# Kernel optimization log

Measured on AMD Instinct MI355X. Metric: run time of the kernel, lower is better.

The kernel has to match this reference:

```python
import jax, jax.numpy as jnp
import numpy as np

B, NQ, NK, QS, KS, H, VD = 16, 64, 512, 256, 256, 256, 256


def setup_inputs() -> dict:
    key = jax.random.key(0)
    k1, k2, k3, k4, k5, k6, k7 = jax.random.split(key, 7)
    return {
        "queries": jax.random.normal(k1, (B, NQ, QS), dtype=jnp.float32),
        "keys": jax.random.normal(k2, (B, NK, KS), dtype=jnp.float32),
        "values": jax.random.normal(k3, (B, NK, VD), dtype=jnp.float32),
        "valid_lens": jax.random.randint(k4, (B,), 1, NK + 1, dtype=jnp.int32),
        # learned params (nn.Linear with bias=False): W_q [QS,H], W_k [KS,H], w_v [H]
        "W_q": jax.random.normal(k5, (QS, H), dtype=jnp.float32) / np.sqrt(QS),
        "W_k": jax.random.normal(k6, (KS, H), dtype=jnp.float32) / np.sqrt(KS),
        "w_v": jax.random.normal(k7, (H,), dtype=jnp.float32) / np.sqrt(H),
    }


def reference(queries, keys, values, valid_lens, W_q, W_k, w_v):
    # project: q [B,nq,H], k [B,nk,H]
    q = jnp.einsum("bqd,dh->bqh", queries, W_q)
    k = jnp.einsum("bkd,dh->bkh", keys, W_k)
    # broadcast-add -> tanh -> score reduction via w_v: [B,nq,nk]
    features = jnp.tanh(q[:, :, None, :] + k[:, None, :, :])  # [B,nq,nk,H]
    scores = jnp.einsum("bqkh,h->bqk", features, w_v)
    # masked softmax over keys (positions >= valid_len masked out)
    mask = jnp.arange(scores.shape[-1])[None, None, :] < valid_lens[:, None, None]
    scores = jnp.where(mask, scores, -1e6)
    attn = jax.nn.softmax(scores, axis=-1)
    # weighted sum of values (dropout p=0 / eval mode => identity)
    return jnp.einsum("bqk,bkv->bqv", attn, values)
```

## Files before the change

kernel.cpp:

```cpp
#include <hip/hip_runtime.h>
#include <hip/hip_bf16.h>

#define BB 16
#define NQ 64
#define NK 512
#define HD 256

typedef __attribute__((ext_vector_type(8))) short short8;
typedef __attribute__((ext_vector_type(4))) float f32x4;

__device__ __forceinline__ ushort bf16_rne(float v) {
    unsigned u = __float_as_uint(v);
    return (ushort)((u + 0x7FFFu + ((u >> 16) & 1u)) >> 16);
}
__device__ __forceinline__ float bf16_to_f(ushort h) {
    return __uint_as_float(((unsigned)h) << 16);
}

__global__ __launch_bounds__(256) void convert_split(
    const float* __restrict__ q, const float* __restrict__ k,
    const float* __restrict__ wq, const float* __restrict__ wk,
    ushort* __restrict__ qh, ushort* __restrict__ ql,
    ushort* __restrict__ kh, ushort* __restrict__ kl,
    ushort* __restrict__ wqh, ushort* __restrict__ wql,
    ushort* __restrict__ wkh, ushort* __restrict__ wkl)
{
    const int idx = blockIdx.x * 256 + threadIdx.x;
    if (blockIdx.x < 2304) {
        int e = idx * 4;
        const float* src; ushort *dh, *dl; int off;
        if (e < 1024 * 256) { src = q; dh = qh; dl = ql; off = e; }
        else { src = k; dh = kh; dl = kl; off = e - 1024 * 256; }
        float4 v = *(const float4*)&src[off];
        float fv[4] = {v.x, v.y, v.z, v.w};
        ushort hh[4], ll[4];
        #pragma unroll
        for (int c = 0; c < 4; ++c) {
            hh[c] = bf16_rne(fv[c]);
            ll[c] = bf16_rne(fv[c] - bf16_to_f(hh[c]));
        }
        *(ushort4*)&dh[off] = make_ushort4(hh[0], hh[1], hh[2], hh[3]);
        *(ushort4*)&dl[off] = make_ushort4(ll[0], ll[1], ll[2], ll[3]);
    } else {
        int widx = idx - 2304 * 256;
        const float* W; ushort *wh, *wl;
        if (widx < 16384) { W = wq; wh = wqh; wl = wql; }
        else { W = wk; wh = wkh; wl = wkl; widx -= 16384; }
        int n  = widx >> 6;
        int k4 = (widx & 63) * 4;
        ushort hh[4], ll[4];
        #pragma unroll
        for (int c = 0; c < 4; ++c) {
            float v = W[(k4 + c) * 256 + n];
            hh[c] = bf16_rne(v);
            ll[c] = bf16_rne(v - bf16_to_f(hh[c]));
        }
        *(ushort4*)&wh[n * 256 + k4] = make_ushort4(hh[0], hh[1], hh[2], hh[3]);
        *(ushort4*)&wl[n * 256 + k4] = make_ushort4(ll[0], ll[1], ll[2], ll[3]);
    }
}

__global__ __launch_bounds__(256, 2) void proj_mfma2(
    const ushort* __restrict__ qh, const ushort* __restrict__ ql,
    const ushort* __restrict__ kh, const ushort* __restrict__ kl,
    const ushort* __restrict__ wqh, const ushort* __restrict__ wql,
    const ushort* __restrict__ wkh, const ushort* __restrict__ wkl,
    float* __restrict__ qp, float* __restrict__ kp, float scale)
{
    __shared__ ushort AsH[128 * 64], AsL[128 * 64];
    __shared__ ushort BsH[64 * 64],  BsL[64 * 64];

    const ushort *Ah, *Al, *Bh, *Bl; float* C; int rows0;
    if (blockIdx.x < 8) { Ah = qh; Al = ql; Bh = wqh; Bl = wql; C = qp; rows0 = blockIdx.x * 128; }
    else                { Ah = kh; Al = kl; Bh = wkh; Bl = wkl; C = kp; rows0 = (blockIdx.x - 8) * 128; }
    const int cols0 = blockIdx.y * 64;

    const int t = threadIdx.x, lane = t & 63, wave = t >> 6;
    const int quad = lane >> 4, l15 = lane & 15;
    const int lr = lane >> 3;
    const int cg = (lane & 7) ^ lr;
    const int swz0 = quad ^ (l15 & 7);
    const int swz1 = (quad + 4) ^ (l15 & 7);

    f32x4 acc[2][4];
    #pragma unroll
    for (int i = 0; i < 2; ++i)
        #pragma unroll
        for (int j = 0; j < 4; ++j)
            acc[i][j] = (f32x4){0.f, 0.f, 0.f, 0.f};

    short8 rAh[4], rAl[4], rBh[2], rBl[2];
    #pragma unroll
    for (int i = 0; i < 4; ++i) {
        size_t g = (size_t)(rows0 + (wave * 4 + i) * 8 + lr) * 256 + cg * 8;
        rAh[i] = *(const short8*)&Ah[g];
        rAl[i] = *(const short8*)&Al[g];
    }
    #pragma unroll
    for (int j = 0; j < 2; ++j) {
        size_t g = (size_t)(cols0 + (wave * 2 + j) * 8 + lr) * 256 + cg * 8;
        rBh[j] = *(const short8*)&Bh[g];
        rBl[j] = *(const short8*)&Bl[g];
    }

    for (int k0 = 0; k0 < 256; k0 += 64) {
        __syncthreads();
        #pragma unroll
        for (int i = 0; i < 4; ++i) {
            int ci = (wave * 4 + i) * 64 + lane;
            *(short8*)&AsH[ci * 8] = rAh[i];
            *(short8*)&AsL[ci * 8] = rAl[i];
        }
        #pragma unroll
        for (int j = 0; j < 2; ++j) {
            int ci = (wave * 2 + j) * 64 + lane;
            *(short8*)&BsH[ci * 8] = rBh[j];
            *(short8*)&BsL[ci * 8] = rBl[j];
        }
        __syncthreads();

        if (k0 + 64 < 256) {
            #pragma unroll
            for (int i = 0; i < 4; ++i) {
                size_t g = (size_t)(rows0 + (wave * 4 + i) * 8 + lr) * 256 + k0 + 64 + cg * 8;
                rAh[i] = *(const short8*)&Ah[g];
                rAl[i] = *(const short8*)&Al[g];
            }
            #pragma unroll
            for (int j = 0; j < 2; ++j) {
                size_t g = (size_t)(cols0 + (wave * 2 + j) * 8 + lr) * 256 + k0 + 64 + cg * 8;
                rBh[j] = *(const short8*)&Bh[g];
                rBl[j] = *(const short8*)&Bl[g];
            }
        }

        #pragma unroll
        for (int ks = 0; ks < 2; ++ks) {
            const int s = ks ? swz1 : swz0;
            short8 aH[2], aL[2], bH[4], bL[4];
            #pragma unroll
            for (int ms = 0; ms < 2; ++ms) {
                int r = wave * 32 + ms * 16 + l15;
                aH[ms] = *(const short8*)&AsH[r * 64 + s * 8];
                aL[ms] = *(const short8*)&AsL[r * 64 + s * 8];
            }
            #pragma unroll
            for (int ns = 0; ns < 4; ++ns) {
                int n = ns * 16 + l15;
                bH[ns] = *(const short8*)&BsH[n * 64 + s * 8];
                bL[ns] = *(const short8*)&BsL[n * 64 + s * 8];
            }
            #pragma unroll
            for (int ms = 0; ms < 2; ++ms)
                #pragma unroll
                for (int ns = 0; ns < 4; ++ns)
                    acc[ms][ns] = __builtin_amdgcn_mfma_f32_16x16x32_bf16(aH[ms], bH[ns], acc[ms][ns], 0, 0, 0);
            #pragma unroll
            for (int ms = 0; ms < 2; ++ms)
                #pragma unroll
                for (int ns = 0; ns < 4; ++ns)
                    acc[ms][ns] = __builtin_amdgcn_mfma_f32_16x16x32_bf16(aL[ms], bH[ns], acc[ms][ns], 0, 0, 0);
            #pragma unroll
            for (int ms = 0; ms < 2; ++ms)
                #pragma unroll
                for (int ns = 0; ns < 4; ++ns)
                    acc[ms][ns] = __builtin_amdgcn_mfma_f32_16x16x32_bf16(aH[ms], bL[ns], acc[ms][ns], 0, 0, 0);
        }
    }

    #pragma unroll
    for (int ms = 0; ms < 2; ++ms) {
        int rbase = rows0 + wave * 32 + ms * 16 + quad * 4;
        #pragma unroll
        for (int ns = 0; ns < 4; ++ns) {
            int col = cols0 + ns * 16 + l15;
            #pragma unroll
            for (int r = 0; r < 4; ++r)
                C[(size_t)(rbase + r) * 256 + col] = acc[ms][ns][r] * scale;
        }
    }
}

__global__ __launch_bounds__(256, 2) void attn_kernel(
    const float* __restrict__ qp,
    const float* __restrict__ kp,
    const float* __restrict__ values,
    const int*   __restrict__ vlens,
    const float* __restrict__ w_v,
    float* __restrict__ out)
{
    __shared__ float q_s[2][HD];
    __shared__ float wv_s[HD];
    __shared__ float sc[2][NK];
    __shared__ float part[4][2][HD];
    __shared__ float redm[4], reds[4], invs[2];

    const int b     = blockIdx.x & 15;
    const int qpair = blockIdx.x >> 4;
    const int qi0   = qpair * 2;
    const int t     = threadIdx.x;
    const int lane  = t & 63;
    const int wave  = t >> 6;
    const int vl    = vlens[b];
    const int vla   = (vl + 15) & ~15;
    const size_t row0 = (size_t)b * NQ + qi0;

    q_s[0][t] = qp[row0 * HD + t];
    q_s[1][t] = qp[(row0 + 1) * HD + t];
    wv_s[t]   = w_v[t];
    __syncthreads();

    float Wsum;
    {
        float ws = wv_s[lane] + wv_s[lane + 64] + wv_s[lane + 128] + wv_s[lane + 192];
        #pragma unroll
        for (int off = 32; off; off >>= 1) ws += __shfl_xor(ws, off);
        Wsum = ws;
    }

    const int keyLoc = lane >> 4;
    const int ch     = lane & 15;
    float4 qa[4], qb[4], wf[4];
    #pragma unroll
    for (int m = 0; m < 4; ++m) {
        qa[m] = *(const float4*)&q_s[0][ch * 4 + m * 64];
        qb[m] = *(const float4*)&q_s[1][ch * 4 + m * 64];
        wf[m] = *(const float4*)&wv_s[ch * 4 + m * 64];
    }

    const float* kbase = kp + (size_t)b * NK * HD;
    const float* kptr  = kbase + (size_t)(wave * 4 + keyLoc) * HD + ch * 4;

    float4 kk[4];
    #pragma unroll
    for (int m = 0; m < 4; ++m) kk[m] = *(const float4*)(kptr + m * 64);

    for (int nb = wave * 4; nb < vla; nb += 16) {
        float4 kn[4];
        #pragma unroll
        for (int m = 0; m < 4; ++m) kn[m] = *(const float4*)(kptr + 16 * HD + m * 64);

        float p0 = 0.f, p1 = 0.f;
        #pragma unroll
        for (int m = 0; m < 4; ++m) {
            float kv[4]  = {kk[m].x, kk[m].y, kk[m].z, kk[m].w};
            float qav[4] = {qa[m].x, qa[m].y, qa[m].z, qa[m].w};
            float qbv[4] = {qb[m].x, qb[m].y, qb[m].z, qb[m].w};
            float wv4[4] = {wf[m].x, wf[m].y, wf[m].z, wf[m].w};
            #pragma unroll
            for (int c = 0; c < 4; ++c) {
                float r0 = __builtin_amdgcn_rcpf(__builtin_amdgcn_exp2f(qav[c] + kv[c]) + 1.f);
                float r1 = __builtin_amdgcn_rcpf(__builtin_amdgcn_exp2f(qbv[c] + kv[c]) + 1.f);
                p0 = fmaf(wv4[c], r0, p0);
                p1 = fmaf(wv4[c], r1, p1);
            }
        }
        p0 += __shfl_down(p0, 8); p0 += __shfl_down(p0, 4);
        p0 += __shfl_down(p0, 2); p0 += __shfl_down(p0, 1);
        p1 += __shfl_down(p1, 8); p1 += __shfl_down(p1, 4);
        p1 += __shfl_down(p1, 2); p1 += __shfl_down(p1, 1);
        if (ch == 0) {
            sc[0][nb + keyLoc] = fmaf(-2.f, p0, Wsum);
            sc[1][nb + keyLoc] = fmaf(-2.f, p1, Wsum);
        }
        #pragma unroll
        for (int m = 0; m < 4; ++m) kk[m] = kn[m];
        kptr += 16 * HD;
    }
    __syncthreads();

    {
        const int qq  = wave >> 1;
        const int sub = wave & 1;
        float m = -1e30f;
        for (int n = sub * 64 + lane; n < vl; n += 128) m = fmaxf(m, sc[qq][n]);
        #pragma unroll
        for (int off = 32; off; off >>= 1) m = fmaxf(m, __shfl_xor(m, off));
        if (lane == 0) redm[wave] = m;
        __syncthreads();
        m = fmaxf(redm[qq * 2], redm[qq * 2 + 1]);

        float ssum = 0.f;
        const float L2E = 1.4426950408889634f;
        for (int n = sub * 64 + lane; n < vl; n += 128) {
            float p = __builtin_amdgcn_exp2f((sc[qq][n] - m) * L2E);
            sc[qq][n] = p;
            ssum += p;
        }
        #pragma unroll
        for (int off = 32; off; off >>= 1) ssum += __shfl_xor(ssum, off);
        if (lane == 0) reds[wave] = ssum;
        if (vl + t < vla) { sc[0][vl + t] = 0.f; sc[1][vl + t] = 0.f; }
        __syncthreads();
        if (t == 0)  invs[0] = __builtin_amdgcn_rcpf(reds[0] + reds[1]);
        if (t == 64) invs[1] = __builtin_amdgcn_rcpf(reds[2] + reds[3]);
    }
    __syncthreads();

    float4 acc0 = {0.f, 0.f, 0.f, 0.f};
    float4 acc1 = {0.f, 0.f, 0.f, 0.f};
    const float* vbase = values + (size_t)b * NK * HD;
    for (int nb = wave * 4; nb < vla; nb += 16) {
        float4 v[4]; float pa[4], pb[4];
        #pragma unroll
        for (int u = 0; u < 4; ++u) {
            v[u]  = *(const float4*)&vbase[(size_t)(nb + u) * HD + lane * 4];
            pa[u] = sc[0][nb + u];
            pb[u] = sc[1][nb + u];
        }
        #pragma unroll
        for (int u = 0; u < 4; ++u) {
            acc0.x = fmaf(pa[u], v[u].x, acc0.x);
            acc0.y = fmaf(pa[u], v[u].y, acc0.y);
            acc0.z = fmaf(pa[u], v[u].z, acc0.z);
            acc0.w = fmaf(pa[u], v[u].w, acc0.w);
            acc1.x = fmaf(pb[u], v[u].x, acc1.x);
            acc1.y = fmaf(pb[u], v[u].y, acc1.y);
            acc1.z = fmaf(pb[u], v[u].z, acc1.z);
            acc1.w = fmaf(pb[u], v[u].w, acc1.w);
        }
    }
    *(float4*)&part[wave][0][lane * 4] = acc0;
    *(float4*)&part[wave][1][lane * 4] = acc1;
    __syncthreads();

    if (wave < 2) {
        float4 p0 = *(const float4*)&part[0][wave][lane * 4];
        float4 p1 = *(const float4*)&part[1][wave][lane * 4];
        float4 p2 = *(const float4*)&part[2][wave][lane * 4];
        float4 p3 = *(const float4*)&part[3][wave][lane * 4];
        const float inv = invs[wave];
        float4 o;
        o.x = ((p0.x + p1.x) + (p2.x + p3.x)) * inv;
        o.y = ((p0.y + p1.y) + (p2.y + p3.y)) * inv;
        o.z = ((p0.z + p1.z) + (p2.z + p3.z)) * inv;
        o.w = ((p0.w + p1.w) + (p2.w + p3.w)) * inv;
        *(float4*)&out[(row0 + wave) * HD + lane * 4] = o;
    }
}

extern "C" void kernel_launch(void* const* d_in, const int* in_sizes, int n_in,
                              void* d_out, int out_size, void* d_ws, size_t ws_size,
                              hipStream_t stream) {
    const float* queries = (const float*)d_in[0];
    const float* keys    = (const float*)d_in[1];
    const float* values  = (const float*)d_in[2];
    const int*   vlens   = (const int*)d_in[3];
    const float* W_q     = (const float*)d_in[4];
    const float* W_k     = (const float*)d_in[5];
    const float* w_v     = (const float*)d_in[6];
    float* out = (float*)d_out;

    float*  kp  = (float*)d_ws;
    ushort* qh  = (ushort*)((char*)d_ws + (8 << 20));
    ushort* ql  = qh  + 1024 * 256;
    ushort* kh  = ql  + 1024 * 256;
    ushort* kl  = kh  + 8192 * 256;
    ushort* wqh = kl  + 8192 * 256;
    ushort* wql = wqh + 65536;
    ushort* wkh = wql + 65536;
    ushort* wkl = wkh + 65536;

    float* qp = out;

    const float SC = 2.885390081777927f;

    convert_split<<<dim3(2432), 256, 0, stream>>>(queries, keys, W_q, W_k,
                                                  qh, ql, kh, kl,
                                                  wqh, wql, wkh, wkl);
    proj_mfma2<<<dim3(72, 4), 256, 0, stream>>>(qh, ql, kh, kl,
                                                wqh, wql, wkh, wkl,
                                                qp, kp, SC);
    attn_kernel<<<dim3(512), 256, 0, stream>>>(qp, kp, values, vlens, w_v, out);
}
```

Before: 119.6 us.

## Split fused attention into tiled score kernel and separate softmax-PV kernel

The score computation moves out of the per-query-pair attention kernel into its own kernel. Each block of that kernel stages 32 queries and 16 keys in shared memory, so each key row is reused across many queries and the 3D grid skips chunks beyond the valid length. Scores go through a global workspace buffer, and a second kernel does the masked softmax and value weighting. This trades an extra launch plus a global round-trip of the score matrix for better key reuse and more parallelism in the tanh-dominated stage.

```diff
diff --git a/kernel.cpp b/kernel.cpp
--- a/kernel.cpp
+++ b/kernel.cpp
@@ -181,16 +181,91 @@
     }
 }
 
-__global__ __launch_bounds__(256, 2) void attn_kernel(
+__global__ __launch_bounds__(256) void score_kernel(
     const float* __restrict__ qp,
     const float* __restrict__ kp,
+    const int*   __restrict__ vlens,
+    const float* __restrict__ w_v,
+    float* __restrict__ S)
+{
+    __shared__ float qs[32][260];
+    __shared__ float ks[16][260];
+    __shared__ float wv[HD];
+
+    const int b     = blockIdx.x;
+    const int chunk = blockIdx.y;
+    const int qhalf = blockIdx.z;
+    const int vl    = vlens[b];
+    if (chunk * 16 >= vl) return;
+
+    const int t    = threadIdx.x;
+    const int lane = t & 63;
+    const int wave = t >> 6;
+
+    const float* qsrc = qp + ((size_t)b * NQ + qhalf * 32) * HD;
+    #pragma unroll
+    for (int i = 0; i < 8; ++i) {
+        int idx = i * 256 + t;
+        int row = idx >> 6, c4 = (idx & 63) * 4;
+        *(float4*)&qs[row][c4] = *(const float4*)&qsrc[(size_t)row * HD + c4];
+    }
+    const float* ksrc = kp + ((size_t)b * NK + chunk * 16) * HD;
+    #pragma unroll
+    for (int i = 0; i < 4; ++i) {
+        int idx = i * 256 + t;
+        int row = idx >> 6, c4 = (idx & 63) * 4;
+        *(float4*)&ks[row][c4] = *(const float4*)&ksrc[(size_t)row * HD + c4];
+    }
+    if (t < 64) *(float4*)&wv[t * 4] = *(const float4*)&w_v[t * 4];
+    __syncthreads();
+
+    float Wsum;
+    {
+        float ws = wv[lane] + wv[lane + 64] + wv[lane + 128] + wv[lane + 192];
+        #pragma unroll
+        for (int off = 32; off; off >>= 1) ws += __shfl_xor(ws, off);
+        Wsum = ws;
+    }
+
+    const int qloc = wave * 8 + (lane >> 3);
+    const int n0   = (lane & 7) * 2;
+
+    const float* qrow = &qs[qloc][0];
+    const float* k0   = &ks[n0][0];
+    const float* k1   = &ks[n0 + 1][0];
+
+    float s0 = 0.f, s1 = 0.f;
+    #pragma unroll 8
+    for (int h4 = 0; h4 < 64; ++h4) {
+        float4 q4 = *(const float4*)&qrow[h4 * 4];
+        float4 w4 = *(const float4*)&wv[h4 * 4];
+        float4 ka = *(const float4*)&k0[h4 * 4];
+        float4 kb = *(const float4*)&k1[h4 * 4];
+        float qv[4] = {q4.x, q4.y, q4.z, q4.w};
+        float wv4[4] = {w4.x, w4.y, w4.z, w4.w};
+        float kav[4] = {ka.x, ka.y, ka.z, ka.w};
+        float kbv[4] = {kb.x, kb.y, kb.z, kb.w};
+        #pragma unroll
+        for (int c = 0; c < 4; ++c) {
+            float r0 = __builtin_amdgcn_rcpf(__builtin_amdgcn_exp2f(qv[c] + kav[c]) + 1.f);
+            float r1 = __builtin_amdgcn_rcpf(__builtin_amdgcn_exp2f(qv[c] + kbv[c]) + 1.f);
+            s0 = fmaf(wv4[c], r0, s0);
+            s1 = fmaf(wv4[c], r1, s1);
+        }
+    }
+    float2 o;
+    o.x = fmaf(-2.f, s0, Wsum);
+    o.y = fmaf(-2.f, s1, Wsum);
+    const int qg = qhalf * 32 + qloc;
+    *(float2*)&S[((size_t)b * NQ + qg) * NK + chunk * 16 + n0] = o;
+}
+
+__global__ __launch_bounds__(256, 2) void softmax_pv(
+    const float* __restrict__ S,
     const float* __restrict__ values,
     const int*   __restrict__ vlens,
-    const float* __restrict__ w_v,
     float* __restrict__ out)
 {
-    __shared__ float q_s[2][HD];
-    __shared__ float wv_s[HD];
     __shared__ float sc[2][NK];
     __shared__ float part[4][2][HD];
     __shared__ float redm[4], reds[4], invs[2];
@@ -205,68 +280,9 @@
     const int vla   = (vl + 15) & ~15;
     const size_t row0 = (size_t)b * NQ + qi0;
 
-    q_s[0][t] = qp[row0 * HD + t];
-    q_s[1][t] = qp[(row0 + 1) * HD + t];
-    wv_s[t]   = w_v[t];
-    __syncthreads();
-
-    float Wsum;
-    {
-        float ws = wv_s[lane] + wv_s[lane + 64] + wv_s[lane + 128] + wv_s[lane + 192];
-        #pragma unroll
-        for (int off = 32; off; off >>= 1) ws += __shfl_xor(ws, off);
-        Wsum = ws;
-    }
-
-    const int keyLoc = lane >> 4;
-    const int ch     = lane & 15;
-    float4 qa[4], qb[4], wf[4];
-    #pragma unroll
-    for (int m = 0; m < 4; ++m) {
-        qa[m] = *(const float4*)&q_s[0][ch * 4 + m * 64];
-        qb[m] = *(const float4*)&q_s[1][ch * 4 + m * 64];
-        wf[m] = *(const float4*)&wv_s[ch * 4 + m * 64];
-    }
-
-    const float* kbase = kp + (size_t)b * NK * HD;
-    const float* kptr  = kbase + (size_t)(wave * 4 + keyLoc) * HD + ch * 4;
-
-    float4 kk[4];
-    #pragma unroll
-    for (int m = 0; m < 4; ++m) kk[m] = *(const float4*)(kptr + m * 64);
-
-    for (int nb = wave * 4; nb < vla; nb += 16) {
-        float4 kn[4];
-        #pragma unroll
-        for (int m = 0; m < 4; ++m) kn[m] = *(const float4*)(kptr + 16 * HD + m * 64);
-
-        float p0 = 0.f, p1 = 0.f;
-        #pragma unroll
-        for (int m = 0; m < 4; ++m) {
-            float kv[4]  = {kk[m].x, kk[m].y, kk[m].z, kk[m].w};
-            float qav[4] = {qa[m].x, qa[m].y, qa[m].z, qa[m].w};
-            float qbv[4] = {qb[m].x, qb[m].y, qb[m].z, qb[m].w};
-            float wv4[4] = {wf[m].x, wf[m].y, wf[m].z, wf[m].w};
-            #pragma unroll
-            for (int c = 0; c < 4; ++c) {
-                float r0 = __builtin_amdgcn_rcpf(__builtin_amdgcn_exp2f(qav[c] + kv[c]) + 1.f);
-                float r1 = __builtin_amdgcn_rcpf(__builtin_amdgcn_exp2f(qbv[c] + kv[c]) + 1.f);
-                p0 = fmaf(wv4[c], r0, p0);
-                p1 = fmaf(wv4[c], r1, p1);
-            }
-        }
-        p0 += __shfl_down(p0, 8); p0 += __shfl_down(p0, 4);
-        p0 += __shfl_down(p0, 2); p0 += __shfl_down(p0, 1);
-        p1 += __shfl_down(p1, 8); p1 += __shfl_down(p1, 4);
-        p1 += __shfl_down(p1, 2); p1 += __shfl_down(p1, 1);
-        if (ch == 0) {
-            sc[0][nb + keyLoc] = fmaf(-2.f, p0, Wsum);
-            sc[1][nb + keyLoc] = fmaf(-2.f, p1, Wsum);
-        }
-        #pragma unroll
-        for (int m = 0; m < 4; ++m) kk[m] = kn[m];
-        kptr += 16 * HD;
-    }
+    const float* S0 = &S[row0 * NK];
+    const float* S1 = &S[(row0 + 1) * NK];
+    for (int n = t; n < vla; n += 256) { sc[0][n] = S0[n]; sc[1][n] = S1[n]; }
     __syncthreads();
 
     {
@@ -352,7 +368,9 @@
     float* out = (float*)d_out;
 
     float*  kp  = (float*)d_ws;
-    ushort* qh  = (ushort*)((char*)d_ws + (8 << 20));
+    float*  qp  = kp + (size_t)BB * NK * HD;
+    float*  S   = qp + (size_t)BB * NQ * HD;
+    ushort* qh  = (ushort*)(S + (size_t)BB * NQ * NK);
     ushort* ql  = qh  + 1024 * 256;
     ushort* kh  = ql  + 1024 * 256;
     ushort* kl  = kh  + 8192 * 256;
@@ -361,8 +379,6 @@
     ushort* wkh = wql + 65536;
     ushort* wkl = wkh + 65536;
 
-    float* qp = out;
-
     const float SC = 2.885390081777927f;
 
     convert_split<<<dim3(2432), 256, 0, stream>>>(queries, keys, W_q, W_k,
@@ -371,5 +387,6 @@
     proj_mfma2<<<dim3(72, 4), 256, 0, stream>>>(qh, ql, kh, kl,
                                                 wqh, wql, wkh, wkl,
                                                 qp, kp, SC);
-    attn_kernel<<<dim3(512), 256, 0, stream>>>(qp, kp, values, vlens, w_v, out);
-}
+    score_kernel<<<dim3(16, 32, 2), 256, 0, stream>>>(qp, kp, vlens, w_v, S);
+    softmax_pv<<<dim3(512), 256, 0, stream>>>(S, values, vlens, out);
+}
```

New measurement: 127.6 us. 1.07x slower.

## Split attention over key segments with split-K softmax combine kernel

Applied to the files above, without the earlier changes.

The single attention kernel becomes two. The first computes scores, a local softmax and the P·V product for each 64-key segment, launching grid (512,8) and skipping segments beyond valid_len. A second kernel merges the per-segment max, sum and partial outputs into the final result. The score math also precomputes exp2(q) once and uses exp2(q)*exp2(k) per element, which removes one add per element but keeps the exp of k per pair. The aim is more parallelism and an even load across blocks with varying valid_len, at the cost of an extra launch and a round trip of the partial outputs through memory.

```diff
diff --git a/kernel.cpp b/kernel.cpp
--- a/kernel.cpp
+++ b/kernel.cpp
@@ -181,147 +181,122 @@
     }
 }
 
-__global__ __launch_bounds__(256, 2) void attn_kernel(
+__global__ __launch_bounds__(256) void score_pv_seg(
     const float* __restrict__ qp,
     const float* __restrict__ kp,
     const float* __restrict__ values,
     const int*   __restrict__ vlens,
     const float* __restrict__ w_v,
-    float* __restrict__ out)
+    float* __restrict__ pO,
+    float* __restrict__ pM,
+    float* __restrict__ pL)
 {
-    __shared__ float q_s[2][HD];
-    __shared__ float wv_s[HD];
-    __shared__ float sc[2][NK];
+    __shared__ float Ps[2][64];
     __shared__ float part[4][2][HD];
-    __shared__ float redm[4], reds[4], invs[2];
 
     const int b     = blockIdx.x & 15;
     const int qpair = blockIdx.x >> 4;
-    const int qi0   = qpair * 2;
-    const int t     = threadIdx.x;
-    const int lane  = t & 63;
-    const int wave  = t >> 6;
+    const int seg   = blockIdx.y;
     const int vl    = vlens[b];
-    const int vla   = (vl + 15) & ~15;
-    const size_t row0 = (size_t)b * NQ + qi0;
-
-    q_s[0][t] = qp[row0 * HD + t];
-    q_s[1][t] = qp[(row0 + 1) * HD + t];
-    wv_s[t]   = w_v[t];
-    __syncthreads();
-
-    float Wsum;
-    {
-        float ws = wv_s[lane] + wv_s[lane + 64] + wv_s[lane + 128] + wv_s[lane + 192];
-        #pragma unroll
-        for (int off = 32; off; off >>= 1) ws += __shfl_xor(ws, off);
-        Wsum = ws;
-    }
-
-    const int keyLoc = lane >> 4;
-    const int ch     = lane & 15;
-    float4 qa[4], qb[4], wf[4];
+    if (seg * 64 >= vl) return;
+
+    const int t = threadIdx.x, lane = t & 63, wave = t >> 6;
+    const int keyLoc = lane >> 4, ch = lane & 15;
+
+    const float* q0 = qp + ((size_t)b * NQ + qpair * 2) * HD;
+    float eqa[16], eqb[16];
+    float4 wf[4];
+    float Wsum = 0.f;
     #pragma unroll
     for (int m = 0; m < 4; ++m) {
-        qa[m] = *(const float4*)&q_s[0][ch * 4 + m * 64];
-        qb[m] = *(const float4*)&q_s[1][ch * 4 + m * 64];
-        wf[m] = *(const float4*)&wv_s[ch * 4 + m * 64];
-    }
-
-    const float* kbase = kp + (size_t)b * NK * HD;
-    const float* kptr  = kbase + (size_t)(wave * 4 + keyLoc) * HD + ch * 4;
-
-    float4 kk[4];
-    #pragma unroll
-    for (int m = 0; m < 4; ++m) kk[m] = *(const float4*)(kptr + m * 64);
-
-    for (int nb = wave * 4; nb < vla; nb += 16) {
-        float4 kn[4];
-        #pragma unroll
-        for (int m = 0; m < 4; ++m) kn[m] = *(const float4*)(kptr + 16 * HD + m * 64);
-
-        float p0 = 0.f, p1 = 0.f;
+        float4 a  = *(const float4*)&q0[ch * 4 + m * 64];
+        float4 bq = *(const float4*)&q0[HD + ch * 4 + m * 64];
+        wf[m] = *(const float4*)&w_v[ch * 4 + m * 64];
+        eqa[m * 4 + 0] = __builtin_amdgcn_exp2f(a.x);
+        eqa[m * 4 + 1] = __builtin_amdgcn_exp2f(a.y);
+        eqa[m * 4 + 2] = __builtin_amdgcn_exp2f(a.z);
+        eqa[m * 4 + 3] = __builtin_amdgcn_exp2f(a.w);
+        eqb[m * 4 + 0] = __builtin_amdgcn_exp2f(bq.x);
+        eqb[m * 4 + 1] = __builtin_amdgcn_exp2f(bq.y);
+        eqb[m * 4 + 2] = __builtin_amdgcn_exp2f(bq.z);
+        eqb[m * 4 + 3] = __builtin_amdgcn_exp2f(bq.w);
+        Wsum += (wf[m].x + wf[m].y) + (wf[m].z + wf[m].w);
+    }
+    Wsum += __shfl_xor(Wsum, 1);
+    Wsum += __shfl_xor(Wsum, 2);
+    Wsum += __shfl_xor(Wsum, 4);
+    Wsum += __shfl_xor(Wsum, 8);
+
+    const float* kbase = kp + ((size_t)b * NK + seg * 64) * HD;
+    #pragma unroll
+    for (int it = 0; it < 4; ++it) {
+        const int nloc = it * 16 + wave * 4 + keyLoc;
+        const float* krow = kbase + (size_t)nloc * HD + ch * 4;
+        float4 kk[4];
+        #pragma unroll
+        for (int m = 0; m < 4; ++m) kk[m] = *(const float4*)&krow[m * 64];
+
+        float s0 = 0.f, s1 = 0.f;
         #pragma unroll
         for (int m = 0; m < 4; ++m) {
             float kv[4]  = {kk[m].x, kk[m].y, kk[m].z, kk[m].w};
-            float qav[4] = {qa[m].x, qa[m].y, qa[m].z, qa[m].w};
-            float qbv[4] = {qb[m].x, qb[m].y, qb[m].z, qb[m].w};
             float wv4[4] = {wf[m].x, wf[m].y, wf[m].z, wf[m].w};
             #pragma unroll
             for (int c = 0; c < 4; ++c) {
-                float r0 = __builtin_amdgcn_rcpf(__builtin_amdgcn_exp2f(qav[c] + kv[c]) + 1.f);
-                float r1 = __builtin_amdgcn_rcpf(__builtin_amdgcn_exp2f(qbv[c] + kv[c]) + 1.f);
-                p0 = fmaf(wv4[c], r0, p0);
-                p1 = fmaf(wv4[c], r1, p1);
-            }
-        }
-        p0 += __shfl_down(p0, 8); p0 += __shfl_down(p0, 4);
-        p0 += __shfl_down(p0, 2); p0 += __shfl_down(p0, 1);
-        p1 += __shfl_down(p1, 8); p1 += __shfl_down(p1, 4);
-        p1 += __shfl_down(p1, 2); p1 += __shfl_down(p1, 1);
+                float ek = __builtin_amdgcn_exp2f(kv[c]);
+                float r0 = __builtin_amdgcn_rcpf(fmaf(eqa[m * 4 + c], ek, 1.f));
+                float r1 = __builtin_amdgcn_rcpf(fmaf(eqb[m * 4 + c], ek, 1.f));
+                s0 = fmaf(wv4[c], r0, s0);
+                s1 = fmaf(wv4[c], r1, s1);
+            }
+        }
+        s0 += __shfl_xor(s0, 1); s0 += __shfl_xor(s0, 2);
+        s0 += __shfl_xor(s0, 4); s0 += __shfl_xor(s0, 8);
+        s1 += __shfl_xor(s1, 1); s1 += __shfl_xor(s1, 2);
+        s1 += __shfl_xor(s1, 4); s1 += __shfl_xor(s1, 8);
         if (ch == 0) {
-            sc[0][nb + keyLoc] = fmaf(-2.f, p0, Wsum);
-            sc[1][nb + keyLoc] = fmaf(-2.f, p1, Wsum);
-        }
-        #pragma unroll
-        for (int m = 0; m < 4; ++m) kk[m] = kn[m];
-        kptr += 16 * HD;
+            const bool masked = (seg * 64 + nloc >= vl);
+            Ps[0][nloc] = masked ? -1e6f : fmaf(-2.f, s0, Wsum);
+            Ps[1][nloc] = masked ? -1e6f : fmaf(-2.f, s1, Wsum);
+        }
     }
     __syncthreads();
 
-    {
-        const int qq  = wave >> 1;
-        const int sub = wave & 1;
-        float m = -1e30f;
-        for (int n = sub * 64 + lane; n < vl; n += 128) m = fmaxf(m, sc[qq][n]);
+    const float L2E = 1.4426950408889634f;
+    if (wave < 2) {
+        float s = Ps[wave][lane];
+        float m = s;
         #pragma unroll
         for (int off = 32; off; off >>= 1) m = fmaxf(m, __shfl_xor(m, off));
-        if (lane == 0) redm[wave] = m;
-        __syncthreads();
-        m = fmaxf(redm[qq * 2], redm[qq * 2 + 1]);
-
-        float ssum = 0.f;
-        const float L2E = 1.4426950408889634f;
-        for (int n = sub * 64 + lane; n < vl; n += 128) {
-            float p = __builtin_amdgcn_exp2f((sc[qq][n] - m) * L2E);
-            sc[qq][n] = p;
-            ssum += p;
-        }
-        #pragma unroll
-        for (int off = 32; off; off >>= 1) ssum += __shfl_xor(ssum, off);
-        if (lane == 0) reds[wave] = ssum;
-        if (vl + t < vla) { sc[0][vl + t] = 0.f; sc[1][vl + t] = 0.f; }
-        __syncthreads();
-        if (t == 0)  invs[0] = __builtin_amdgcn_rcpf(reds[0] + reds[1]);
-        if (t == 64) invs[1] = __builtin_amdgcn_rcpf(reds[2] + reds[3]);
+        float e = __builtin_amdgcn_exp2f((s - m) * L2E);
+        float l = e;
+        #pragma unroll
+        for (int off = 32; off; off >>= 1) l += __shfl_xor(l, off);
+        Ps[wave][lane] = e;
+        if (lane == 0) {
+            size_t mi = ((size_t)(b * 32 + qpair) * 8 + seg) * 2 + wave;
+            pM[mi] = m;
+            pL[mi] = l;
+        }
     }
     __syncthreads();
 
-    float4 acc0 = {0.f, 0.f, 0.f, 0.f};
-    float4 acc1 = {0.f, 0.f, 0.f, 0.f};
-    const float* vbase = values + (size_t)b * NK * HD;
-    for (int nb = wave * 4; nb < vla; nb += 16) {
-        float4 v[4]; float pa[4], pb[4];
-        #pragma unroll
-        for (int u = 0; u < 4; ++u) {
-            v[u]  = *(const float4*)&vbase[(size_t)(nb + u) * HD + lane * 4];
-            pa[u] = sc[0][nb + u];
-            pb[u] = sc[1][nb + u];
-        }
-        #pragma unroll
-        for (int u = 0; u < 4; ++u) {
-            acc0.x = fmaf(pa[u], v[u].x, acc0.x);
-            acc0.y = fmaf(pa[u], v[u].y, acc0.y);
-            acc0.z = fmaf(pa[u], v[u].z, acc0.z);
-            acc0.w = fmaf(pa[u], v[u].w, acc0.w);
-            acc1.x = fmaf(pb[u], v[u].x, acc1.x);
-            acc1.y = fmaf(pb[u], v[u].y, acc1.y);
-            acc1.z = fmaf(pb[u], v[u].z, acc1.z);
-            acc1.w = fmaf(pb[u], v[u].w, acc1.w);
-        }
-    }
-    *(float4*)&part[wave][0][lane * 4] = acc0;
-    *(float4*)&part[wave][1][lane * 4] = acc1;
+    f32x4 acc0 = (f32x4){0.f, 0.f, 0.f, 0.f};
+    f32x4 acc1 = (f32x4){0.f, 0.f, 0.f, 0.f};
+    const float* vbase = values + ((size_t)b * NK + seg * 64) * HD;
+    #pragma unroll
+    for (int i = 0; i < 16; ++i) {
+        const int k = wave * 16 + i;
+        float p0 = Ps[0][k];
+        float p1 = Ps[1][k];
+        float4 v = *(const float4*)&vbase[(size_t)k * HD + lane * 4];
+        acc0[0] = fmaf(p0, v.x, acc0[0]); acc0[1] = fmaf(p0, v.y, acc0[1]);
+        acc0[2] = fmaf(p0, v.z, acc0[2]); acc0[3] = fmaf(p0, v.w, acc0[3]);
+        acc1[0] = fmaf(p1, v.x, acc1[0]); acc1[1] = fmaf(p1, v.y, acc1[1]);
+        acc1[2] = fmaf(p1, v.z, acc1[2]); acc1[3] = fmaf(p1, v.w, acc1[3]);
+    }
+    *(f32x4*)&part[wave][0][lane * 4] = acc0;
+    *(f32x4*)&part[wave][1][lane * 4] = acc1;
     __syncthreads();
 
     if (wave < 2) {
@@ -329,14 +304,55 @@
         float4 p1 = *(const float4*)&part[1][wave][lane * 4];
         float4 p2 = *(const float4*)&part[2][wave][lane * 4];
         float4 p3 = *(const float4*)&part[3][wave][lane * 4];
-        const float inv = invs[wave];
-        float4 o;
-        o.x = ((p0.x + p1.x) + (p2.x + p3.x)) * inv;
-        o.y = ((p0.y + p1.y) + (p2.y + p3.y)) * inv;
-        o.z = ((p0.z + p1.z) + (p2.z + p3.z)) * inv;
-        o.w = ((p0.w + p1.w) + (p2.w + p3.w)) * inv;
-        *(float4*)&out[(row0 + wave) * HD + lane * 4] = o;
-    }
+        f32x4 o;
+        o[0] = (p0.x + p1.x) + (p2.x + p3.x);
+        o[1] = (p0.y + p1.y) + (p2.y + p3.y);
+        o[2] = (p0.z + p1.z) + (p2.z + p3.z);
+        o[3] = (p0.w + p1.w) + (p2.w + p3.w);
+        size_t ob = (((size_t)(b * 32 + qpair) * 8 + seg) * 2 + wave) * 256;
+        *(f32x4*)&pO[ob + lane * 4] = o;
+    }
+}
+
+__global__ __launch_bounds__(256) void combine_seg(
+    const float* __restrict__ pO, const float* __restrict__ pM,
+    const float* __restrict__ pL, const int* __restrict__ vlens,
+    float* __restrict__ out)
+{
+    const int b  = blockIdx.x >> 6;
+    const int q  = blockIdx.x & 63;
+    const int t  = threadIdx.x;
+    const int vl = vlens[b];
+    const int nc = (vl + 63) >> 6;
+    const int qpair = q >> 1, q2 = q & 1;
+    const float L2E = 1.4426950408889634f;
+
+    const size_t base = (size_t)(b * 32 + qpair) * 8;
+
+    float mi[8], li[8];
+    float m = -3e38f;
+    #pragma unroll
+    for (int i = 0; i < 8; ++i) {
+        if (i < nc) {
+            mi[i] = pM[(base + i) * 2 + q2];
+            li[i] = pL[(base + i) * 2 + q2];
+            m = fmaxf(m, mi[i]);
+        }
+    }
+    float L = 0.f, wi[8];
+    #pragma unroll
+    for (int i = 0; i < 8; ++i) {
+        if (i < nc) {
+            wi[i] = __builtin_amdgcn_exp2f((mi[i] - m) * L2E);
+            L = fmaf(li[i], wi[i], L);
+        }
+    }
+    float acc = 0.f;
+    #pragma unroll
+    for (int i = 0; i < 8; ++i) {
+        if (i < nc) acc = fmaf(wi[i], pO[((base + i) * 2 + q2) * 256 + t], acc);
+    }
+    out[((size_t)(b * 64 + q)) * 256 + t] = acc * __builtin_amdgcn_rcpf(L);
 }
 
 extern "C" void kernel_launch(void* const* d_in, const int* in_sizes, int n_in,
@@ -352,7 +368,11 @@
     float* out = (float*)d_out;
 
     float*  kp  = (float*)d_ws;
-    ushort* qh  = (ushort*)((char*)d_ws + (8 << 20));
+    float*  qp  = kp + (size_t)BB * NK * HD;
+    float*  pO  = qp + (size_t)BB * NQ * HD;
+    float*  pM  = pO + (size_t)BB * 32 * 8 * 2 * 256;
+    float*  pL  = pM + (size_t)BB * 32 * 8 * 2;
+    ushort* qh  = (ushort*)(pL + (size_t)BB * 32 * 8 * 2);
     ushort* ql  = qh  + 1024 * 256;
     ushort* kh  = ql  + 1024 * 256;
     ushort* kl  = kh  + 8192 * 256;
@@ -361,8 +381,6 @@
     ushort* wkh = wql + 65536;
     ushort* wkl = wkh + 65536;
 
-    float* qp = out;
-
     const float SC = 2.885390081777927f;
 
     convert_split<<<dim3(2432), 256, 0, stream>>>(queries, keys, W_q, W_k,
@@ -371,5 +389,7 @@
     proj_mfma2<<<dim3(72, 4), 256, 0, stream>>>(qh, ql, kh, kl,
                                                 wqh, wql, wkh, wkl,
                                                 qp, kp, SC);
-    attn_kernel<<<dim3(512), 256, 0, stream>>>(qp, kp, values, vlens, w_v, out);
-}
+    score_pv_seg<<<dim3(512, 8), 256, 0, stream>>>(qp, kp, values, vlens, w_v,
+                                                   pO, pM, pL);
+    combine_seg<<<dim3(BB * NQ), 256, 0, stream>>>(pO, pM, pL, vlens, out);
+}
```

After: 120.2 us. Within noise of the previous version (+0.5%).
